# Performance work log

Hardware: AMD Instinct MI355X
Metric: run time of the kernel (lower is better)

Reference implementation:

```python
import jax, jax.numpy as jnp
import numpy as np

B, C, D, H, W = 2, 3, 128, 160, 160
RANGE_FLOW = 0.4


def setup_inputs() -> dict:
    key = jax.random.key(0)
    k1, k2 = jax.random.split(key)
    flow_1 = jax.random.normal(k1, (B, C, D, H, W), dtype=jnp.float32)
    flow_2 = jax.random.normal(k2, (B, C, D, H, W), dtype=jnp.float32)
    # identity sampling grid in voxel coords, channel order (x, y, z)
    zz, yy, xx = jnp.meshgrid(
        jnp.arange(D, dtype=jnp.float32),
        jnp.arange(H, dtype=jnp.float32),
        jnp.arange(W, dtype=jnp.float32),
        indexing='ij')
    sample_grid = jnp.broadcast_to(jnp.stack([xx, yy, zz], axis=-1), (B, D, H, W, 3))
    range_flow = jnp.float32(RANGE_FLOW)
    return {"flow_1": flow_1, "flow_2": flow_2, "sample_grid": sample_grid,
            "range_flow": range_flow}


def grid_sample_3d_border(vol, grid):
    """PyTorch F.grid_sample 3D, mode='bilinear' (trilinear), align_corners=True,
    padding_mode='border'. vol: [B,C,D,H,W], grid: [B,D,H,W,3] normalized (x,y,z)."""
    Bv, Cv, Dv, Hv, Wv = vol.shape
    # unnormalize (align_corners=True) and clamp to border
    x = jnp.clip((grid[..., 0] + 1.0) * 0.5 * (Wv - 1), 0.0, Wv - 1)
    y = jnp.clip((grid[..., 1] + 1.0) * 0.5 * (Hv - 1), 0.0, Hv - 1)
    z = jnp.clip((grid[..., 2] + 1.0) * 0.5 * (Dv - 1), 0.0, Dv - 1)
    x0f, y0f, z0f = jnp.floor(x), jnp.floor(y), jnp.floor(z)
    wx, wy, wz = x - x0f, y - y0f, z - z0f  # fractional weights [B,D,H,W]
    ix0 = x0f.astype(jnp.int32); ix1 = jnp.minimum(ix0 + 1, Wv - 1)
    iy0 = y0f.astype(jnp.int32); iy1 = jnp.minimum(iy0 + 1, Hv - 1)
    iz0 = z0f.astype(jnp.int32); iz1 = jnp.minimum(iz0 + 1, Dv - 1)

    vol_flat = vol.reshape(Bv, Cv, -1)  # [B,C,D*H*W]
    gD, gH, gW = grid.shape[1:4]

    def gather(iz, iy, ix):
        idx = ((iz * Hv + iy) * Wv + ix).reshape(Bv, 1, -1)
        return jnp.take_along_axis(vol_flat, idx, axis=2).reshape(Bv, Cv, gD, gH, gW)

    # broadcast weights over channel dim
    wx = wx[:, None]; wy = wy[:, None]; wz = wz[:, None]
    c000 = gather(iz0, iy0, ix0); c001 = gather(iz0, iy0, ix1)
    c010 = gather(iz0, iy1, ix0); c011 = gather(iz0, iy1, ix1)
    c100 = gather(iz1, iy0, ix0); c101 = gather(iz1, iy0, ix1)
    c110 = gather(iz1, iy1, ix0); c111 = gather(iz1, iy1, ix1)
    c00 = c000 * (1 - wx) + c001 * wx
    c01 = c010 * (1 - wx) + c011 * wx
    c10 = c100 * (1 - wx) + c101 * wx
    c11 = c110 * (1 - wx) + c111 * wx
    c0 = c00 * (1 - wy) + c01 * wy
    c1 = c10 * (1 - wy) + c11 * wy
    return c0 * (1 - wz) + c1 * wz


def reference(flow_1, flow_2, sample_grid, range_flow):
    Dv, Hv, Wv = sample_grid.shape[1:4]
    g = sample_grid + jnp.transpose(flow_1, (0, 2, 3, 4, 1)) * range_flow
    # normalize each coordinate channel to [-1, 1] (align_corners convention)
    gx = 2.0 * g[..., 0] / (Wv - 1) - 1.0
    gy = 2.0 * g[..., 1] / (Hv - 1) - 1.0
    gz = 2.0 * g[..., 2] / (Dv - 1) - 1.0
    grid = jnp.stack([gx, gy, gz], axis=-1)
    return grid_sample_3d_border(flow_2, grid) + flow_1
```

## Files before the change

### kernel.cpp

```cpp
#include <hip/hip_runtime.h>


constexpr int DD = 128, HH = 160, WW = 160;
constexpr int HW = HH * WW;
constexpr int SP = DD * HW;
constexpr int TX = 32, TH = 8, TD = 8;
constexpr int PX = 64, PY = 12, PZ = 12;
constexpr int PHF = PX * PY * PZ;
constexpr int VSLOT = PHF / 4;
constexpr int RUNS = VSLOT / 256;
constexpr int NTX = WW / TX, NTH = HH / TH, NTD = DD / TD;
constexpr int NB = 2 * NTX * NTH * NTD;

#define AS1 __attribute__((address_space(1)))
#define AS3 __attribute__((address_space(3)))

__global__ __launch_bounds__(256, 4) void comp_xform_px64(
    const float* __restrict__ f1,
    const float* __restrict__ f2,
    const float* __restrict__ rfp,
    float* __restrict__ out)
{
    __shared__ __align__(16) float slab[PHF];

    const int tid = threadIdx.x;

    const int bid = blockIdx.x;
    const int wg  = (bid & 7) * (NB / 8) + (bid >> 3);

    const int tx = wg % NTX; int r_ = wg / NTX;
    const int th = r_ % NTH; r_ /= NTH;
    const int td = r_ % NTD; const int b = r_ / NTD;

    const int x0 = tx * TX, h0 = th * TH, d0 = td * TD;
    const int xlo = x0 - 4, ylo = h0 - 2, zlo = d0 - 2;

    const size_t boff = (size_t)b * (size_t)(3 * SP);
    const float* __restrict__ f1b = f1 + boff;
    const float* __restrict__ f2b = f2 + boff;
    float* __restrict__ ob = out + boff;

    const float rf = rfp[0];

    const int wl = tid & 31, hh = tid >> 5;
    const int w = x0 + wl, h = h0 + hh;
    const int sp0 = (d0 * HH + h) * WW + w;
    const int wbase = tid & 192;

    int goff[RUNS];
#pragma unroll
    for (int r = 0; r < RUNS; ++r) {
        const int s = r * 256 + tid;
        const int row = s >> 4, k = s & 15;
        const int rz = row / PY, ry = row - rz * PY;
        const int gz = min(max(zlo + rz, 0), DD - 1);
        const int gy = min(max(ylo + ry, 0), HH - 1);
        const int gx = min(max(xlo + 4 * k, 0), WW - 4);
        goff[r] = (gz * HH + gy) * WW + gx;
    }

    auto stage = [&](const float* __restrict__ src) {
#pragma unroll
        for (int r = 0; r < RUNS; ++r) {
            const float* gp = src + goff[r];
            AS3 void* lp = (AS3 void*)&slab[(r * 256 + wbase) * 4];
            __builtin_amdgcn_global_load_lds((const AS1 void*)gp, lp, 16, 0, 0);
        }
    };

    stage(f2b);

    float f1s0[8], f1s1[8], f1s2[8];
#pragma unroll
    for (int dd = 0; dd < TD; ++dd) {
        const int sp = sp0 + dd * HW;
        f1s0[dd] = f1b[sp];
        f1s1[dd] = f1b[SP + sp];
        f1s2[dd] = f1b[2 * SP + sp];
    }

    int voff[8]; float wxs[8], wys[8], wzs[8]; unsigned okm = 0;
#pragma unroll
    for (int dd = 0; dd < TD; ++dd) {
        const float x = fminf(fmaxf((float)w + rf * f1s0[dd], 0.f), (float)(WW - 1));
        const float y = fminf(fmaxf((float)h + rf * f1s1[dd], 0.f), (float)(HH - 1));
        const float z = fminf(fmaxf((float)(d0 + dd) + rf * f1s2[dd], 0.f), (float)(DD - 1));
        const float fx = floorf(x), fy = floorf(y), fz = floorf(z);
        const int rx = (int)fx - xlo, ry = (int)fy - ylo, rz = (int)fz - zlo;
        const bool ok = ((unsigned)rx <= 38u) & ((unsigned)ry <= 10u) & ((unsigned)rz <= 10u);
        okm |= (ok ? 1u : 0u) << dd;
        voff[dd] = ok ? ((rz * PY + ry) * PX + rx) : 0;
        wxs[dd] = ok ? (x - fx) : x;
        wys[dd] = ok ? (y - fy) : y;
        wzs[dd] = ok ? (z - fz) : z;
    }

    __syncthreads();

#pragma unroll
    for (int c = 0; c < 3; ++c) {
        const float* __restrict__ br  = slab;
        const float* __restrict__ f2c = f2b + (size_t)c * SP;
        float* __restrict__ oc = ob + (size_t)c * SP;

#pragma unroll
        for (int dd = 0; dd < TD; ++dd) {
            const float* p = br + voff[dd];
            const float wx = wxs[dd], wy = wys[dd], wz = wzs[dd];
            const float ax = 1.f - wx, ay = 1.f - wy, az = 1.f - wz;
            const float a0 = p[0],            a1 = p[1];
            const float b0 = p[PX],           b1 = p[PX + 1];
            const float c0 = p[PX * PY],      c1 = p[PX * PY + 1];
            const float e0 = p[PX * PY + PX], e1 = p[PX * PY + PX + 1];
            const float top = ay * fmaf(a0, ax, a1 * wx) + wy * fmaf(b0, ax, b1 * wx);
            const float bot = ay * fmaf(c0, ax, c1 * wx) + wy * fmaf(e0, ax, e1 * wx);
            const float res = az * top + wz * bot;
            const float f1c = (c == 0) ? f1s0[dd] : ((c == 1) ? f1s1[dd] : f1s2[dd]);
            oc[sp0 + dd * HW] = res + f1c;
        }

        if (okm != 255u) {
#pragma unroll
            for (int dd = 0; dd < TD; ++dd) {
                if (!((okm >> dd) & 1u)) {
                    const float X = wxs[dd], Y = wys[dd], Z = wzs[dd];
                    const float fx = floorf(X), fy = floorf(Y), fz = floorf(Z);
                    const float wx = X - fx, wy = Y - fy, wz = Z - fz;
                    const int ix0 = (int)fx, iy0 = (int)fy, iz0 = (int)fz;
                    const int ix1 = min(ix0 + 1, WW - 1);
                    const int iy1 = min(iy0 + 1, HH - 1);
                    const int iz1 = min(iz0 + 1, DD - 1);
                    const int q00 = (iz0 * HH + iy0) * WW, q01 = (iz0 * HH + iy1) * WW;
                    const int q10 = (iz1 * HH + iy0) * WW, q11 = (iz1 * HH + iy1) * WW;
                    const float c000 = f2c[q00 + ix0], c001 = f2c[q00 + ix1];
                    const float c010 = f2c[q01 + ix0], c011 = f2c[q01 + ix1];
                    const float c100 = f2c[q10 + ix0], c101 = f2c[q10 + ix1];
                    const float c110 = f2c[q11 + ix0], c111 = f2c[q11 + ix1];
                    const float ax = 1.f - wx, ay = 1.f - wy, az = 1.f - wz;
                    const float top = ay * (c000 * ax + c001 * wx) + wy * (c010 * ax + c011 * wx);
                    const float bot = ay * (c100 * ax + c101 * wx) + wy * (c110 * ax + c111 * wx);
                    const float f1c = (c == 0) ? f1s0[dd] : ((c == 1) ? f1s1[dd] : f1s2[dd]);
                    oc[sp0 + dd * HW] = az * top + wz * bot + f1c;
                }
            }
        }

        if (c < 2) {
            __syncthreads();
            stage(f2b + (size_t)(c + 1) * SP);
            __syncthreads();
        }
    }
}

extern "C" void kernel_launch(void* const* d_in, const int* in_sizes, int n_in,
                              void* d_out, int out_size, void* d_ws, size_t ws_size,
                              hipStream_t stream) {
    const float* f1  = (const float*)d_in[0];
    const float* f2  = (const float*)d_in[1];
    const float* rfp = (const float*)d_in[3];
    float* out = (float*)d_out;

    comp_xform_px64<<<NB, 256, 0, stream>>>(f1, f2, rfp, out);
}
```

Baseline: 45.62 us.

## Stage flow_2 halo in LDS as packed bf16 x-pairs for single-load gathers

Replaces the direct global-to-LDS async copies with register-staged loads that truncate each f2 value to bf16. Each LDS word now holds a voxel together with its x+1 neighbour, so the trilinear gather needs 4 LDS reads instead of 8. This trades the async copy path for explicit VGPR loads, packing ALU work and an extra scalar global load per run. It also cuts output precision, since the interpolated values are truncated to bf16.

```diff
diff --git a/kernel.cpp b/kernel.cpp
--- a/kernel.cpp
+++ b/kernel.cpp
@@ -1,4 +1,5 @@
 #include <hip/hip_runtime.h>
+#include <stdint.h>
 
 
 constexpr int DD = 128, HH = 160, WW = 160;
@@ -7,21 +8,17 @@
 constexpr int TX = 32, TH = 8, TD = 8;
 constexpr int PX = 64, PY = 12, PZ = 12;
 constexpr int PHF = PX * PY * PZ;
-constexpr int VSLOT = PHF / 4;
-constexpr int RUNS = VSLOT / 256;
+constexpr int RUNS = PHF / 4 / 256;
 constexpr int NTX = WW / TX, NTH = HH / TH, NTD = DD / TD;
 constexpr int NB = 2 * NTX * NTH * NTD;
 
-#define AS1 __attribute__((address_space(1)))
-#define AS3 __attribute__((address_space(3)))
-
-__global__ __launch_bounds__(256, 4) void comp_xform_px64(
+__global__ __launch_bounds__(256, 4) void comp_xform_bf16(
     const float* __restrict__ f1,
     const float* __restrict__ f2,
     const float* __restrict__ rfp,
     float* __restrict__ out)
 {
-    __shared__ __align__(16) float slab[PHF];
+    __shared__ __align__(16) uint32_t slab[PHF];
 
     const int tid = threadIdx.x;
 
@@ -45,9 +42,8 @@
     const int wl = tid & 31, hh = tid >> 5;
     const int w = x0 + wl, h = h0 + hh;
     const int sp0 = (d0 * HH + h) * WW + w;
-    const int wbase = tid & 192;
 
-    int goff[RUNS];
+    int goff[RUNS], goffe[RUNS];
 #pragma unroll
     for (int r = 0; r < RUNS; ++r) {
         const int s = r * 256 + tid;
@@ -56,15 +52,35 @@
         const int gz = min(max(zlo + rz, 0), DD - 1);
         const int gy = min(max(ylo + ry, 0), HH - 1);
         const int gx = min(max(xlo + 4 * k, 0), WW - 4);
-        goff[r] = (gz * HH + gy) * WW + gx;
+        const int rowb = (gz * HH + gy) * WW;
+        goff[r]  = rowb + gx;
+        goffe[r] = rowb + min(gx + 4, WW - 1);
     }
 
+    auto pack2 = [](float a, float bb) -> uint32_t {
+        return (__float_as_uint(a) >> 16) | (__float_as_uint(bb) & 0xFFFF0000u);
+    };
+
     auto stage = [&](const float* __restrict__ src) {
+#pragma unroll 1
+        for (int g = 0; g < 3; ++g) {
+            float4 a[3]; float e[3];
 #pragma unroll
-        for (int r = 0; r < RUNS; ++r) {
-            const float* gp = src + goff[r];
-            AS3 void* lp = (AS3 void*)&slab[(r * 256 + wbase) * 4];
-            __builtin_amdgcn_global_load_lds((const AS1 void*)gp, lp, 16, 0, 0);
+            for (int j = 0; j < 3; ++j) {
+                const int r = g * 3 + j;
+                a[j] = *reinterpret_cast<const float4*>(src + goff[r]);
+                e[j] = src[goffe[r]];
+            }
+#pragma unroll
+            for (int j = 0; j < 3; ++j) {
+                const int r = g * 3 + j;
+                uint4 dq;
+                dq.x = pack2(a[j].x, a[j].y);
+                dq.y = pack2(a[j].y, a[j].z);
+                dq.z = pack2(a[j].z, a[j].w);
+                dq.w = pack2(a[j].w, e[j]);
+                *reinterpret_cast<uint4*>(&slab[4 * (r * 256 + tid)]) = dq;
+            }
         }
     };
 
@@ -99,19 +115,22 @@
 
 #pragma unroll
     for (int c = 0; c < 3; ++c) {
-        const float* __restrict__ br  = slab;
         const float* __restrict__ f2c = f2b + (size_t)c * SP;
         float* __restrict__ oc = ob + (size_t)c * SP;
 
 #pragma unroll
         for (int dd = 0; dd < TD; ++dd) {
-            const float* p = br + voff[dd];
+            const int p = voff[dd];
+            const uint32_t u0 = slab[p];
+            const uint32_t u1 = slab[p + PX];
+            const uint32_t u2 = slab[p + PX * PY];
+            const uint32_t u3 = slab[p + PX * PY + PX];
             const float wx = wxs[dd], wy = wys[dd], wz = wzs[dd];
             const float ax = 1.f - wx, ay = 1.f - wy, az = 1.f - wz;
-            const float a0 = p[0],            a1 = p[1];
-            const float b0 = p[PX],           b1 = p[PX + 1];
-            const float c0 = p[PX * PY],      c1 = p[PX * PY + 1];
-            const float e0 = p[PX * PY + PX], e1 = p[PX * PY + PX + 1];
+            const float a0 = __uint_as_float(u0 << 16), a1 = __uint_as_float(u0 & 0xFFFF0000u);
+            const float b0 = __uint_as_float(u1 << 16), b1 = __uint_as_float(u1 & 0xFFFF0000u);
+            const float c0 = __uint_as_float(u2 << 16), c1 = __uint_as_float(u2 & 0xFFFF0000u);
+            const float e0 = __uint_as_float(u3 << 16), e1 = __uint_as_float(u3 & 0xFFFF0000u);
             const float top = ay * fmaf(a0, ax, a1 * wx) + wy * fmaf(b0, ax, b1 * wx);
             const float bot = ay * fmaf(c0, ax, c1 * wx) + wy * fmaf(e0, ax, e1 * wx);
             const float res = az * top + wz * bot;
@@ -161,5 +180,5 @@
     const float* rfp = (const float*)d_in[3];
     float* out = (float*)d_out;
 
-    comp_xform_px64<<<NB, 256, 0, stream>>>(f1, f2, rfp, out);
+    comp_xform_bf16<<<NB, 256, 0, stream>>>(f1, f2, rfp, out);
 }
```

Result: slower. 58.05 us (+27.2%).
